# Optimization experiments

Measured on AMD Instinct MI355X. Metric: run time of the kernel, lower is better.

Reference implementation:

```python
import jax, jax.numpy as jnp
import numpy as np
from jax import lax

B, T, F = 64, 1536, 512
POOL = 6
UNITS = 256
NUM_CLASSES = 250


def _hard_sigmoid(x):
    # Keras hard_sigmoid: clip(0.2*x + 0.5, 0, 1)
    return jnp.clip(0.2 * x + 0.5, 0.0, 1.0)


def setup_inputs() -> dict:
    key = jax.random.key(0)
    ks = jax.random.split(key, 6)
    x = jax.random.normal(ks[0], (B, T, F), dtype=jnp.float32)
    # ConvLSTM1D with kernel_size=1 over a length-1 spatial axis == dense gates.
    W = jax.random.normal(ks[1], (F, 4 * UNITS), dtype=jnp.float32) * 0.05   # input kernel
    R = jax.random.normal(ks[2], (UNITS, 4 * UNITS), dtype=jnp.float32) * 0.05  # recurrent kernel
    b = jnp.zeros((4 * UNITS,), dtype=jnp.float32)
    Wd = jax.random.normal(ks[3], (UNITS, NUM_CLASSES), dtype=jnp.float32) * 0.05
    bd = jnp.zeros((NUM_CLASSES,), dtype=jnp.float32)
    return {"x": x, "W": W, "R": R, "b": b, "Wd": Wd, "bd": bd}


def reference(x, W, R, b, Wd, bd):
    Bx, Tx, Fx = x.shape
    Tp = Tx // POOL
    # AveragePooling1D(pool_size=6) over time
    xp = x[:, : Tp * POOL].reshape(Bx, Tp, POOL, Fx).mean(axis=2)  # [B, Tp, F]
    # Precompute input-to-gate contribution for all steps (one big GEMM)
    zx = jnp.einsum('btf,fg->btg', xp, W) + b  # [B, Tp, 4U]
    z_seq = jnp.swapaxes(zx, 0, 1)  # [Tp, B, 4U]

    h0 = jnp.zeros((Bx, UNITS), dtype=x.dtype)
    c0 = jnp.zeros((Bx, UNITS), dtype=x.dtype)

    def step(carry, z_t):
        h, c = carry
        z = z_t + h @ R  # [B, 4U]
        i, f, g, o = jnp.split(z, 4, axis=-1)  # Keras gate order: i, f, c, o
        i = _hard_sigmoid(i)
        f = _hard_sigmoid(f)
        g = jnp.tanh(g)
        o = _hard_sigmoid(o)
        c = f * c + i * g
        h = o * jnp.tanh(c)
        return (h, c), None

    (h, _), _ = lax.scan(step, (h0, c0), z_seq)
    # squeeze(-2) + dropout(eval: identity) + flatten -> [B, UNITS]
    logits = h @ Wd + bd
    return jax.nn.softmax(logits, axis=-1)
```

## Files before the change

### kernel.cpp

```cpp
#include <hip/hip_runtime.h>
#include <hip/hip_bf16.h>

#define BB 64
#define TT 1536
#define FF 512
#define TP 256
#define UU 256
#define GG 1024
#define NC 250

typedef _Float16 h2_t __attribute__((ext_vector_type(2)));
typedef _Float16 f16x8 __attribute__((ext_vector_type(8)));
typedef float f32x4 __attribute__((ext_vector_type(4)));

#if defined(__has_builtin)
#  if __has_builtin(__builtin_amdgcn_fdot2)
#    define FDOT2(a, b, c) __builtin_amdgcn_fdot2((a), (b), (c), false)
#  endif
#endif
#ifndef FDOT2
__device__ __forceinline__ float fdot2_fb(h2_t a, h2_t b, float c) {
    return c + (float)a[0] * (float)b[0] + (float)a[1] * (float)b[1];
}
#  define FDOT2(a, b, c) fdot2_fb((a), (b), (c))
#endif

#define BC(u) __builtin_bit_cast(h2_t, (u))

__device__ __forceinline__ float hsig(float z) {
    return fminf(fmaxf(fmaf(z, 0.2f, 0.5f), 0.0f), 1.0f);
}

__device__ __forceinline__ float ftanh(float x) {
    float ax = fabsf(x);
    float e = __expf(-2.0f * ax);
    float t = (1.0f - e) / (1.0f + e);
    return copysignf(t, x);
}

__device__ __forceinline__ void dot4(float& z, const uint4& r, const uint4& h) {
    z = FDOT2(BC(r.x), BC(h.x), z);
    z = FDOT2(BC(r.y), BC(h.y), z);
    z = FDOT2(BC(r.z), BC(h.z), z);
    z = FDOT2(BC(r.w), BC(h.w), z);
}

#if defined(__has_builtin) && __has_builtin(__builtin_amdgcn_mov_dpp)
template <int CTRL>
__device__ __forceinline__ float qperm(float v) {
    return __builtin_bit_cast(float,
        __builtin_amdgcn_mov_dpp(__builtin_bit_cast(int, v), CTRL, 0xf, 0xf, true));
}
#else
template <int CTRL>
__device__ __forceinline__ float qperm(float v) {
    return __shfl_xor(v, CTRL == 0xB1 ? 1 : 2, 64);
}
#endif

__global__ __launch_bounds__(256) void pool_kernel(const float* __restrict__ x,
                                                   _Float16* __restrict__ xph) {
    int idx = blockIdx.x * 256 + threadIdx.x;
    int f = idx & (FF - 1);
    int m = idx >> 9;
    int b = m >> 8;
    int tp = m & (TP - 1);
    const float* src = x + ((size_t)b * TT + (size_t)tp * 6) * FF + f;
    float s = 0.0f;
#pragma unroll
    for (int j = 0; j < 6; ++j) s += src[j * FF];
    xph[idx] = (_Float16)(s * (1.0f / 6.0f));
}

__global__ __launch_bounds__(256) void conv_wt(const float* __restrict__ W,
                                               _Float16* __restrict__ Wt) {
    int d = blockIdx.x * 256 + threadIdx.x;
    int n = d >> 9;
    int k = d & 511;
    Wt[d] = (_Float16)W[(size_t)k * GG + n];
}

__global__ __launch_bounds__(256) void conv_rq(const float* __restrict__ R,
                                               unsigned* __restrict__ Rq) {
    int d = blockIdx.x * 256 + threadIdx.x;
    int i = d & 3;
    int qt = d >> 2;
    int t = qt & 511;
    int q = qt >> 9;
    int g = t >> 2, s = t & 3;
    int c = 8 * g + (q >> 3);
    int p4 = q & 7;
    int k = 64 * s + 8 * p4 + 2 * i;
    h2_t p;
    p[0] = (_Float16)R[(size_t)k * GG + c];
    p[1] = (_Float16)R[(size_t)(k + 1) * GG + c];
    Rq[d] = __builtin_bit_cast(unsigned, p);
}

__global__ __launch_bounds__(256, 2) void gemm_zx_mfma(const _Float16* __restrict__ Ah,
                                                       const _Float16* __restrict__ Bt,
                                                       const float* __restrict__ bias,
                                                       float* __restrict__ C) {
    __shared__ _Float16 As[128 * 40];
    __shared__ _Float16 Bs[128 * 40];
    const int tid = threadIdx.x;
    const int bn = blockIdx.x * 128;
    const int bm = blockIdx.y * 128;
    const int wave = tid >> 6, lane = tid & 63;
    const int wm = (wave & 1) * 64, wn = (wave >> 1) * 64;
    const int l15 = lane & 15, q8 = (lane >> 4) * 8;
    const int srow = tid >> 1, shalf = tid & 1;

    f32x4 acc[4][4] = {};
    const uint4* ag = (const uint4*)(Ah + (size_t)(bm + srow) * FF);
    const uint4* bg = (const uint4*)(Bt + (size_t)(bn + srow) * FF);
    uint4* as_st = (uint4*)As + 5 * srow + 2 * shalf;
    uint4* bs_st = (uint4*)Bs + 5 * srow + 2 * shalf;

    for (int k0 = 0; k0 < FF; k0 += 32) {
        int qi = (k0 >> 3) + shalf * 2;
        uint4 a0 = ag[qi], a1 = ag[qi + 1];
        uint4 b0 = bg[qi], b1 = bg[qi + 1];
        __syncthreads();
        as_st[0] = a0; as_st[1] = a1;
        bs_st[0] = b0; bs_st[1] = b1;
        __syncthreads();
        f16x8 af[4], bf[4];
#pragma unroll
        for (int mt = 0; mt < 4; ++mt)
            af[mt] = *(const f16x8*)&As[(wm + 16 * mt + l15) * 40 + q8];
#pragma unroll
        for (int nt = 0; nt < 4; ++nt)
            bf[nt] = *(const f16x8*)&Bs[(wn + 16 * nt + l15) * 40 + q8];
#pragma unroll
        for (int mt = 0; mt < 4; ++mt)
#pragma unroll
            for (int nt = 0; nt < 4; ++nt)
                acc[mt][nt] = __builtin_amdgcn_mfma_f32_16x16x32_f16(af[mt], bf[nt],
                                                                    acc[mt][nt], 0, 0, 0);
    }
    const int rq = (lane >> 4) * 4;
#pragma unroll
    for (int nt = 0; nt < 4; ++nt) {
        int col = bn + wn + 16 * nt + l15;
        float bv = bias[col];
#pragma unroll
        for (int mt = 0; mt < 4; ++mt) {
#pragma unroll
            for (int r = 0; r < 4; ++r) {
                int row = bm + wm + 16 * mt + rq + r;
                C[(size_t)row * GG + col] = ((const float*)&acc[mt][nt])[r] + bv;
            }
        }
    }
}

__global__ __launch_bounds__(512, 2) void lstm_scan(const float* __restrict__ zx,
                                                    const uint4* __restrict__ Rq4,
                                                    float* __restrict__ hfin) {
    __shared__ uint4 Rl[6][512];
    __shared__ float zfull[GG];
    __shared__ __align__(16) uint4 h2s[36];
    const int b = blockIdx.x;
    const int t = threadIdx.x;
    const int g = t >> 2, s = t & 3;

    uint4 rv[50];
#pragma unroll
    for (int q = 0; q < 50; ++q) rv[q] = Rq4[q * 512 + t];
#pragma unroll
    for (int j = 0; j < 6; ++j) Rl[j][t] = Rq4[(50 + j) * 512 + t];
    if (t < 144) ((unsigned*)h2s)[t] = 0u;
    float c = 0.0f;
    const float* zrow = zx + (size_t)b * TP * GG;
    const uint4* sRq = Rq4 + 56 * 512 + t;
    const uint4* h4 = h2s;
    __syncthreads();

    for (int step = 0; step < TP; ++step) {
        uint4 st[8];
#pragma unroll
        for (int j = 0; j < 8; ++j) st[j] = sRq[j * 512];
        float zxi = 0.f, zxf = 0.f, zxg = 0.f, zxo = 0.f;
        if (t < UU) {
            const float* zr = zrow + (size_t)step * GG;
            zxi = zr[t]; zxf = zr[UU + t]; zxg = zr[2 * UU + t]; zxo = zr[3 * UU + t];
        }

        float z[8] = {};
#pragma unroll
        for (int p4 = 0; p4 < 8; ++p4) {
            uint4 hh = h4[9 * s + p4];
#pragma unroll
            for (int cc = 0; cc < 8; ++cc) {
                int q = cc * 8 + p4;
                if (q < 50)      dot4(z[cc], rv[q], hh);
                else if (q < 56) dot4(z[cc], Rl[q - 50][t], hh);
                else             dot4(z[cc], st[q - 56], hh);
            }
        }
#pragma unroll
        for (int cc = 0; cc < 8; ++cc) {
            z[cc] += qperm<0xB1>(z[cc]);
            z[cc] += qperm<0x4E>(z[cc]);
        }
        float w0 = s == 0 ? z[0] : s == 1 ? z[2] : s == 2 ? z[4] : z[6];
        float w1 = s == 0 ? z[1] : s == 1 ? z[3] : s == 2 ? z[5] : z[7];
        *(float2*)&zfull[8 * g + 2 * s] = make_float2(w0, w1);
        __syncthreads();
        if (t < UU) {
            float zi = zfull[t] + zxi;
            float zf = zfull[UU + t] + zxf;
            float zg = zfull[2 * UU + t] + zxg;
            float zo = zfull[3 * UU + t] + zxo;
            float ig = hsig(zi);
            float fg = hsig(zf);
            float gv = ftanh(zg);
            float og = hsig(zo);
            c = fmaf(fg, c, ig * gv);
            float h = og * ftanh(c);
            int s2 = t >> 6, pos = t & 63;
            ((_Float16*)h2s)[s2 * 72 + pos] = (_Float16)h;
            if (step == TP - 1) hfin[(size_t)b * UU + t] = h;
        }
        __syncthreads();
    }
}

__global__ __launch_bounds__(256) void dense_softmax(const float* __restrict__ hfin,
                                                     const float* __restrict__ Wd,
                                                     const float* __restrict__ bd,
                                                     float* __restrict__ out) {
    __shared__ __align__(16) float hbuf[UU];
    __shared__ float red[256];
    const int b = blockIdx.x;
    const int tid = threadIdx.x;
    hbuf[tid] = hfin[(size_t)b * UU + tid];
    __syncthreads();
    float logit = -3.0e38f;
    if (tid < NC) {
        float acc = bd[tid];
        for (int u = 0; u < UU; u += 4) {
            float4 hv = *(const float4*)&hbuf[u];
            acc = fmaf(hv.x, Wd[(size_t)(u + 0) * NC + tid], acc);
            acc = fmaf(hv.y, Wd[(size_t)(u + 1) * NC + tid], acc);
            acc = fmaf(hv.z, Wd[(size_t)(u + 2) * NC + tid], acc);
            acc = fmaf(hv.w, Wd[(size_t)(u + 3) * NC + tid], acc);
        }
        logit = acc;
    }
    red[tid] = logit;
    __syncthreads();
    for (int s = 128; s > 0; s >>= 1) {
        if (tid < s) red[tid] = fmaxf(red[tid], red[tid + s]);
        __syncthreads();
    }
    float mx = red[0];
    __syncthreads();
    float e = (tid < NC) ? expf(logit - mx) : 0.0f;
    red[tid] = e;
    __syncthreads();
    for (int s = 128; s > 0; s >>= 1) {
        if (tid < s) red[tid] += red[tid + s];
        __syncthreads();
    }
    if (tid < NC) out[(size_t)b * NC + tid] = e / red[0];
}

extern "C" void kernel_launch(void* const* d_in, const int* in_sizes, int n_in,
                              void* d_out, int out_size, void* d_ws, size_t ws_size,
                              hipStream_t stream) {
    const float* x  = (const float*)d_in[0];
    const float* W  = (const float*)d_in[1];
    const float* R  = (const float*)d_in[2];
    const float* bv = (const float*)d_in[3];
    const float* Wd = (const float*)d_in[4];
    const float* bd = (const float*)d_in[5];
    float* out = (float*)d_out;

    char* ws = (char*)d_ws;
    _Float16* xph = (_Float16*)ws;
    float* zx = (float*)(ws + 16777216);
    _Float16* Wt = (_Float16*)(ws + 83886080);
    unsigned* Rq = (unsigned*)(ws + 84934656);
    float* hfin = (float*)(ws + 85458944);

    hipLaunchKernelGGL(pool_kernel, dim3(32768), dim3(256), 0, stream, x, xph);
    hipLaunchKernelGGL(conv_wt, dim3(2048), dim3(256), 0, stream, W, Wt);
    hipLaunchKernelGGL(conv_rq, dim3(512), dim3(256), 0, stream, R, Rq);
    hipLaunchKernelGGL(gemm_zx_mfma, dim3(8, 128), dim3(256), 0, stream,
                       xph, Wt, bv, zx);
    hipLaunchKernelGGL(lstm_scan, dim3(64), dim3(512), 0, stream, zx,
                       (const uint4*)Rq, hfin);
    hipLaunchKernelGGL(dense_softmax, dim3(64), dim3(256), 0, stream, hfin, Wd, bd, out);
}
```

Measured before the change: 765.5 us.

## Remap recurrent weight columns so gate reduction stays in registers, double-buffer h

Recurrent weights are permuted so each quad of threads owns the i/f/g/o columns for two hidden units. The gate nonlinearity and cell update then run directly on the reduced register values, with no trip through a shared zfull array. The h vector is double-buffered in LDS, which removes one of the two block barriers per time step. The register/LDS/streamed split of R changes (42/12/10 instead of 50/6/8), trading register pressure for more LDS and more per-step global reads; half the threads now do the cell math instead of one half-block.

After: 788.8 us. 3.0% more time.

```diff
diff --git a/kernel.cpp b/kernel.cpp
--- a/kernel.cpp
+++ b/kernel.cpp
@@ -8,6 +8,10 @@
 #define UU 256
 #define GG 1024
 #define NC 250
+
+#define RV 42
+#define RLN 12
+#define RST 10
 
 typedef _Float16 h2_t __attribute__((ext_vector_type(2)));
 typedef _Float16 f16x8 __attribute__((ext_vector_type(8)));
@@ -87,13 +91,14 @@
     int qt = d >> 2;
     int t = qt & 511;
     int q = qt >> 9;
-    int g = t >> 2, s = t & 3;
-    int c = 8 * g + (q >> 3);
-    int p4 = q & 7;
+    int s = t & 3, jq = t >> 2;
+    int cc = q >> 3, p4 = q & 7;
+    int g3 = cc >> 1, uo = cc & 1;
+    int col = 256 * g3 + 2 * jq + uo;
     int k = 64 * s + 8 * p4 + 2 * i;
     h2_t p;
-    p[0] = (_Float16)R[(size_t)k * GG + c];
-    p[1] = (_Float16)R[(size_t)(k + 1) * GG + c];
+    p[0] = (_Float16)R[(size_t)k * GG + col];
+    p[1] = (_Float16)R[(size_t)(k + 1) * GG + col];
     Rq[d] = __builtin_bit_cast(unsigned, p);
 }
 
@@ -158,45 +163,46 @@
 __global__ __launch_bounds__(512, 2) void lstm_scan(const float* __restrict__ zx,
                                                     const uint4* __restrict__ Rq4,
                                                     float* __restrict__ hfin) {
-    __shared__ uint4 Rl[6][512];
-    __shared__ float zfull[GG];
-    __shared__ __align__(16) uint4 h2s[36];
+    __shared__ uint4 Rl[RLN][512];
+    __shared__ __align__(16) uint4 h2s[2 * 36];
     const int b = blockIdx.x;
     const int t = threadIdx.x;
-    const int g = t >> 2, s = t & 3;
-
-    uint4 rv[50];
-#pragma unroll
-    for (int q = 0; q < 50; ++q) rv[q] = Rq4[q * 512 + t];
-#pragma unroll
-    for (int j = 0; j < 6; ++j) Rl[j][t] = Rq4[(50 + j) * 512 + t];
-    if (t < 144) ((unsigned*)h2s)[t] = 0u;
+    const int s = t & 3, jq = t >> 2;
+
+    uint4 rv[RV];
+#pragma unroll
+    for (int q = 0; q < RV; ++q) rv[q] = Rq4[q * 512 + t];
+#pragma unroll
+    for (int j = 0; j < RLN; ++j) Rl[j][t] = Rq4[(RV + j) * 512 + t];
+    if (t < 288) ((unsigned*)h2s)[t] = 0u;
     float c = 0.0f;
     const float* zrow = zx + (size_t)b * TP * GG;
-    const uint4* sRq = Rq4 + 56 * 512 + t;
+    const uint4* sRq = Rq4 + (RV + RLN) * 512 + t;
     const uint4* h4 = h2s;
     __syncthreads();
 
     for (int step = 0; step < TP; ++step) {
-        uint4 st[8];
-#pragma unroll
-        for (int j = 0; j < 8; ++j) st[j] = sRq[j * 512];
-        float zxi = 0.f, zxf = 0.f, zxg = 0.f, zxo = 0.f;
-        if (t < UU) {
-            const float* zr = zrow + (size_t)step * GG;
-            zxi = zr[t]; zxf = zr[UU + t]; zxg = zr[2 * UU + t]; zxo = zr[3 * UU + t];
+        const int hb = (step & 1) * 36;
+        const int nb = 36 - hb;
+        uint4 st[RST];
+#pragma unroll
+        for (int j = 0; j < RST; ++j) st[j] = sRq[j * 512];
+        float zv0 = 0.f, zv1 = 0.f, zv2 = 0.f, zv3 = 0.f;
+        if (s < 2) {
+            const float* zr = zrow + (size_t)step * GG + 2 * jq + s;
+            zv0 = zr[0]; zv1 = zr[UU]; zv2 = zr[2 * UU]; zv3 = zr[3 * UU];
         }
 
         float z[8] = {};
 #pragma unroll
         for (int p4 = 0; p4 < 8; ++p4) {
-            uint4 hh = h4[9 * s + p4];
+            uint4 hh = h4[hb + 9 * s + p4];
 #pragma unroll
             for (int cc = 0; cc < 8; ++cc) {
                 int q = cc * 8 + p4;
-                if (q < 50)      dot4(z[cc], rv[q], hh);
-                else if (q < 56) dot4(z[cc], Rl[q - 50][t], hh);
-                else             dot4(z[cc], st[q - 56], hh);
+                if (q < RV)            dot4(z[cc], rv[q], hh);
+                else if (q < RV + RLN) dot4(z[cc], Rl[q - RV][t], hh);
+                else                   dot4(z[cc], st[q - RV - RLN], hh);
             }
         }
 #pragma unroll
@@ -204,24 +210,20 @@
             z[cc] += qperm<0xB1>(z[cc]);
             z[cc] += qperm<0x4E>(z[cc]);
         }
-        float w0 = s == 0 ? z[0] : s == 1 ? z[2] : s == 2 ? z[4] : z[6];
-        float w1 = s == 0 ? z[1] : s == 1 ? z[3] : s == 2 ? z[5] : z[7];
-        *(float2*)&zfull[8 * g + 2 * s] = make_float2(w0, w1);
-        __syncthreads();
-        if (t < UU) {
-            float zi = zfull[t] + zxi;
-            float zf = zfull[UU + t] + zxf;
-            float zg = zfull[2 * UU + t] + zxg;
-            float zo = zfull[3 * UU + t] + zxo;
+        if (s < 2) {
+            float zi = z[0 + s] + zv0;
+            float zf = z[2 + s] + zv1;
+            float zg = z[4 + s] + zv2;
+            float zo = z[6 + s] + zv3;
             float ig = hsig(zi);
             float fg = hsig(zf);
             float gv = ftanh(zg);
             float og = hsig(zo);
             c = fmaf(fg, c, ig * gv);
             float h = og * ftanh(c);
-            int s2 = t >> 6, pos = t & 63;
-            ((_Float16*)h2s)[s2 * 72 + pos] = (_Float16)h;
-            if (step == TP - 1) hfin[(size_t)b * UU + t] = h;
+            int u = 2 * jq + s;
+            ((_Float16*)h2s)[nb * 8 + (u >> 6) * 72 + (u & 63)] = (_Float16)h;
+            if (step == TP - 1) hfin[(size_t)b * UU + u] = h;
         }
         __syncthreads();
     }
@@ -251,8 +253,8 @@
     }
     red[tid] = logit;
     __syncthreads();
-    for (int s = 128; s > 0; s >>= 1) {
-        if (tid < s) red[tid] = fmaxf(red[tid], red[tid + s]);
+    for (int sft = 128; sft > 0; sft >>= 1) {
+        if (tid < sft) red[tid] = fmaxf(red[tid], red[tid + sft]);
         __syncthreads();
     }
     float mx = red[0];
@@ -260,8 +262,8 @@
     float e = (tid < NC) ? expf(logit - mx) : 0.0f;
     red[tid] = e;
     __syncthreads();
-    for (int s = 128; s > 0; s >>= 1) {
-        if (tid < s) red[tid] += red[tid + s];
+    for (int sft = 128; sft > 0; sft >>= 1) {
+        if (tid < sft) red[tid] += red[tid + sft];
         __syncthreads();
     }
     if (tid < NC) out[(size_t)b * NC + tid] = e / red[0];
```
